# Optimization experiments

Hardware: AMD Instinct MI355X
Metric: run time of the kernel (lower is better)

Reference implementation:

```python
import jax, jax.numpy as jnp
import numpy as np

N, E = 50000, 500000
IN_C, HID, OUT_C, HEADS, NL = 128, 16, 16, 8, 4
EPS = 1e-5
NEG_SLOPE = 0.2


def _gatv2(x, src, dst, Wl, Wr, att, bias, concat):
    # GATv2Conv (PyG semantics, eval mode): lin_l on source, lin_r on target,
    # e = a . LeakyReLU(xl[src] + xr[dst]); segment softmax over dst; scatter-sum.
    n = x.shape[0]
    H, C = att.shape
    xl = (x @ Wl).reshape(n, H, C)
    xr = (x @ Wr).reshape(n, H, C)
    e = jax.nn.leaky_relu(xl[src] + xr[dst], NEG_SLOPE)          # [E', H, C]
    logit = jnp.einsum('ehc,hc->eh', e, att)                      # [E', H]
    mx = jax.lax.stop_gradient(jax.ops.segment_max(logit, dst, num_segments=n))
    a = jnp.exp(logit - mx[dst])
    denom = jax.ops.segment_sum(a, dst, num_segments=n)
    alpha = a / denom[dst]                                        # [E', H]
    out = jax.ops.segment_sum(xl[src] * alpha[..., None], dst, num_segments=n)
    out = out.reshape(n, H * C) if concat else out.mean(axis=1)
    return out + bias


def _bn_eval(x, g, b, m, v):
    return (x - m) * jax.lax.rsqrt(v + EPS) * g + b


def setup_inputs() -> dict:
    key = jax.random.key(0)
    ks = jax.random.split(key, 32)
    d = {}
    d['x'] = jax.random.normal(ks[0], (N, IN_C), dtype=jnp.float32)
    d['edge_index'] = jax.random.randint(ks[1], (2, E), 0, N, dtype=jnp.int64)
    HC = HID * HEADS  # 128
    dims_in = [IN_C, HC, HC, HC]
    dims_h = [HEADS, HEADS, HEADS, 1]
    dims_c = [HID, HID, HID, OUT_C]
    ki = 2
    for i in range(NL):
        fan = dims_in[i]
        s = 1.0 / np.sqrt(fan)
        d[f'W{i}l'] = jax.random.uniform(ks[ki], (fan, dims_h[i] * dims_c[i]), minval=-s, maxval=s, dtype=jnp.float32); ki += 1
        d[f'W{i}r'] = jax.random.uniform(ks[ki], (fan, dims_h[i] * dims_c[i]), minval=-s, maxval=s, dtype=jnp.float32); ki += 1
        d[f'a{i}'] = jax.random.normal(ks[ki], (dims_h[i], dims_c[i]), dtype=jnp.float32) * 0.1; ki += 1
        out_dim = dims_h[i] * dims_c[i] if i < NL - 1 else dims_c[i]
        d[f'b{i}'] = jnp.zeros((out_dim,), dtype=jnp.float32)
    for i in range(NL - 1):
        d[f'g{i}'] = jnp.ones((HC,), dtype=jnp.float32) + 0.1 * jax.random.normal(ks[ki], (HC,), dtype=jnp.float32); ki += 1
        d[f'be{i}'] = 0.1 * jax.random.normal(ks[ki], (HC,), dtype=jnp.float32); ki += 1
        d[f'm{i}'] = 0.1 * jax.random.normal(ks[ki], (HC,), dtype=jnp.float32); ki += 1
        d[f'v{i}'] = jnp.ones((HC,), dtype=jnp.float32)
    return d


def reference(x, edge_index, W0l, W0r, a0, b0, W1l, W1r, a1, b1, W2l, W2r, a2, b2, W3l, W3r, a3, b3, g0, be0, m0, v0, g1, be1, m1, v1, g2, be2, m2, v2):
    n = x.shape[0]
    loop = jnp.arange(n, dtype=edge_index.dtype)
    src = jnp.concatenate([edge_index[0], loop])  # add_self_loops=True (PyG default)
    dst = jnp.concatenate([edge_index[1], loop])
    Ws = [(W0l, W0r, a0, b0), (W1l, W1r, a1, b1), (W2l, W2r, a2, b2), (W3l, W3r, a3, b3)]
    bns = [(g0, be0, m0, v0), (g1, be1, m1, v1), (g2, be2, m2, v2)]
    h = x
    for i in range(NL):
        Wl, Wr, att, bias = Ws[i]
        h = _gatv2(h, src, dst, Wl, Wr, att, bias, concat=(i < NL - 1))
        if i < NL - 1:
            g, b, m, v = bns[i]
            h = jax.nn.elu(_bn_eval(h, g, b, m, v))
    return h
```

## Files before the change

kernel.cpp:

```cpp
#include <hip/hip_runtime.h>
#include <hip/hip_fp16.h>
#include <math.h>

static constexpr float BN_EPS = 1e-5f;
static constexpr float NEG = 0.2f;

typedef float f32x4 __attribute__((ext_vector_type(4)));
typedef _Float16 h16x2 __attribute__((ext_vector_type(2)));
typedef _Float16 h16x8 __attribute__((ext_vector_type(8)));


__global__ void hist_kernel(const int* __restrict__ ei, int E, int n, int* __restrict__ cnt) {
    int e = blockIdx.x * blockDim.x + threadIdx.x;
    int ET = E + n;
    if (e >= ET) return;
    int d = (e < E) ? ei[E + e] : (e - E);
    atomicAdd(&cnt[d], 1);
}

__global__ void scan_block(const int* __restrict__ cnt, int* __restrict__ rowptr,
                           int* __restrict__ bsums, int n) {
    __shared__ int s[1024];
    int i = blockIdx.x * 1024 + threadIdx.x;
    int vv = (i < n) ? cnt[i] : 0;
    s[threadIdx.x] = vv;
    __syncthreads();
    for (int d = 1; d < 1024; d <<= 1) {
        int t = (threadIdx.x >= d) ? s[threadIdx.x - d] : 0;
        __syncthreads();
        s[threadIdx.x] += t;
        __syncthreads();
    }
    if (i < n) rowptr[i + 1] = s[threadIdx.x];
    if (threadIdx.x == 1023) bsums[blockIdx.x] = s[1023];
}

__global__ void scan_bsums(int* __restrict__ bsums, int nb) {
    int L = threadIdx.x;
    int v = (L < nb) ? bsums[L] : 0;
    for (int d = 1; d < 64; d <<= 1) {
        int t = __shfl_up(v, d);
        if (L >= d) v += t;
    }
    int ex = __shfl_up(v, 1);
    if (L == 0) ex = 0;
    if (L < nb) bsums[L] = ex;
}

__global__ void scan_add(int* __restrict__ rowptr, const int* __restrict__ bsums, int n) {
    int i = blockIdx.x * 1024 + threadIdx.x;
    if (i < n) rowptr[i + 1] += bsums[blockIdx.x];
    if (i == 0) rowptr[0] = 0;
}

__global__ void scatter_kernel(const int* __restrict__ ei, int E, int n,
                               const int* __restrict__ rowptr, int* __restrict__ fill,
                               int* __restrict__ col) {
    int e = blockIdx.x * blockDim.x + threadIdx.x;
    int ET = E + n;
    if (e >= ET) return;
    int s, d;
    if (e < E) { s = ei[e]; d = ei[E + e]; } else { s = e - E; d = s; }
    int pos = atomicAdd(&fill[d], 1);
    col[rowptr[d] + pos] = s;
}


__global__ void pack_all(const float* __restrict__ W0l, const float* __restrict__ W0r,
                         const float* __restrict__ W1l, const float* __restrict__ W1r,
                         const float* __restrict__ W2l, const float* __restrict__ W2r,
                         const float* __restrict__ W3l, const float* __restrict__ W3r,
                         __half* __restrict__ pk0, __half* __restrict__ pk1,
                         __half* __restrict__ pk2, __half* __restrict__ pk3) {
    int b = blockIdx.x;
    const float *Wl, *Wr;
    __half* packed;
    int tile, NTT, M;
    if (b < 192) {
        int layer = b >> 6;
        tile = b & 63;
        NTT = 16; M = 128;
        Wl = (layer == 0) ? W0l : (layer == 1) ? W1l : W2l;
        Wr = (layer == 0) ? W0r : (layer == 1) ? W1r : W2r;
        packed = (layer == 0) ? pk0 : (layer == 1) ? pk1 : pk2;
    } else {
        tile = b - 192;
        NTT = 2; M = 16;
        Wl = W3l; Wr = W3r; packed = pk3;
    }
    int NT = NTT >> 1;
    int gnt = tile % NTT;
    int kt = tile / NTT;
    int l = threadIdx.x;
    const float* W = (gnt < NT) ? Wl : Wr;
    int col = (gnt % NT) * 16 + (l & 15);
    int krow = kt * 32 + ((l >> 4) << 3);
    size_t base = (size_t)tile * 512 + (size_t)l * 8;
#pragma unroll
    for (int j = 0; j < 8; j++)
        packed[base + j] = __float2half(W[(size_t)(krow + j) * M + col]);
}


template <bool FIRST>
__global__ __launch_bounds__(256) void gemm_h_big(
    const __half* __restrict__ xh, const float* __restrict__ xf,
    const __half* __restrict__ packed,
    __half* __restrict__ Y1, __half* __restrict__ Y2, int n) {
    __shared__ _Float16 sA[64 * 136];
    const int t = threadIdx.x;
    const int row0 = blockIdx.x * 64;

    for (int c = t; c < 1024; c += 256) {
        int row = c >> 4;
        int off = (c & 15) * 8;
        int gr = row0 + row;
        if (gr >= n) gr = n - 1;
        if (FIRST) {
            float4 v0 = *(const float4*)&xf[(size_t)gr * 128 + off];
            float4 v1 = *(const float4*)&xf[(size_t)gr * 128 + off + 4];
            h16x8 h = {(_Float16)v0.x, (_Float16)v0.y, (_Float16)v0.z, (_Float16)v0.w,
                       (_Float16)v1.x, (_Float16)v1.y, (_Float16)v1.z, (_Float16)v1.w};
            *(h16x8*)&sA[row * 136 + off] = h;
        } else {
            *(h16x8*)&sA[row * 136 + off] = *(const h16x8*)&xh[(size_t)gr * 128 + off];
        }
    }
    __syncthreads();

    const int lane = t & 63;
    const int s = t >> 6;
    const int lr = lane & 15;
    const int kq = (lane >> 4) * 8;

    h16x8 af[4][4];
#pragma unroll
    for (int rt = 0; rt < 4; rt++)
#pragma unroll
        for (int kt = 0; kt < 4; kt++)
            af[rt][kt] = *(const h16x8*)&sA[(rt * 16 + lr) * 136 + kt * 32 + kq];

    f32x4 acc[4][4];
#pragma unroll
    for (int a = 0; a < 4; a++)
#pragma unroll
        for (int b = 0; b < 4; b++) acc[a][b] = (f32x4){0.f, 0.f, 0.f, 0.f};

#pragma unroll
    for (int kt = 0; kt < 4; kt++) {
#pragma unroll
        for (int ntl = 0; ntl < 4; ntl++) {
            int nt = s * 4 + ntl;
            h16x8 b = *(const h16x8*)&packed[((size_t)(kt * 16 + nt)) * 512 + lane * 8];
#pragma unroll
            for (int rt = 0; rt < 4; rt++)
                acc[ntl][rt] = __builtin_amdgcn_mfma_f32_16x16x32_f16(af[rt][kt], b, acc[ntl][rt], 0, 0, 0);
        }
    }

    __half* Y = (s < 2) ? Y1 : Y2;
    const int colh = (s & 1) * 64;
    const int rq = (lane >> 4) * 4;
#pragma unroll
    for (int ntl = 0; ntl < 4; ntl++) {
        int col = colh + ntl * 16 + lr;
#pragma unroll
        for (int rt = 0; rt < 4; rt++) {
#pragma unroll
            for (int g = 0; g < 4; g++) {
                int row = row0 + rt * 16 + rq + g;
                if (row < n) Y[(size_t)row * 128 + col] = __float2half(acc[ntl][rt][g]);
            }
        }
    }
}


__global__ __launch_bounds__(256) void gemm_h_small(
    const __half* __restrict__ xh, const __half* __restrict__ packed,
    float* __restrict__ Y1, float* __restrict__ Y2, int n) {
    int lane = threadIdx.x & 63;
    int wv = blockIdx.x * 4 + (threadIdx.x >> 6);
    int row0 = wv * 16;
    if (row0 >= n) return;
    int r = row0 + (lane & 15);
    if (r >= n) r = n - 1;
    int kq = (lane >> 4) * 8;

    h16x8 af[4];
#pragma unroll
    for (int kt = 0; kt < 4; kt++)
        af[kt] = *(const h16x8*)&xh[(size_t)r * 128 + kt * 32 + kq];

    f32x4 acc[2];
    acc[0] = (f32x4){0.f, 0.f, 0.f, 0.f};
    acc[1] = (f32x4){0.f, 0.f, 0.f, 0.f};

#pragma unroll
    for (int kt = 0; kt < 4; kt++) {
#pragma unroll
        for (int nt = 0; nt < 2; nt++) {
            h16x8 b = *(const h16x8*)&packed[((size_t)(kt * 2 + nt)) * 512 + lane * 8];
            acc[nt] = __builtin_amdgcn_mfma_f32_16x16x32_f16(af[kt], b, acc[nt], 0, 0, 0);
        }
    }

    int colb = lane & 15;
    int rbase = row0 + (lane >> 4) * 4;
#pragma unroll
    for (int nt = 0; nt < 2; nt++) {
        float* Y = (nt == 0) ? Y1 : Y2;
#pragma unroll
        for (int g = 0; g < 4; g++) {
            int row = rbase + g;
            if (row < n) Y[(size_t)row * 16 + colb] = acc[nt][g];
        }
    }
}


__device__ __forceinline__ float dot4_h(h16x2 l01, h16x2 l23,
                                        h16x2 a01, h16x2 a23) {
#if __has_builtin(__builtin_amdgcn_fdot2)
    float part = __builtin_amdgcn_fdot2(l01, a01, 0.f, false);
    return __builtin_amdgcn_fdot2(l23, a23, part, false);
#else
    return fmaf((float)l01.x, (float)a01.x, fmaf((float)l01.y, (float)a01.y,
           fmaf((float)l23.x, (float)a23.x, (float)l23.y * (float)a23.y)));
#endif
}

__global__ __launch_bounds__(256) void agg_h(
    const __half* __restrict__ xl, const __half* __restrict__ xr,
    const int* __restrict__ rowptr, const int* __restrict__ col,
    const float* __restrict__ att, const float* __restrict__ bias,
    const float* __restrict__ g, const float* __restrict__ be,
    const float* __restrict__ bm, const float* __restrict__ bv,
    __half* __restrict__ oh, int n) {
    int v = (blockIdx.x * blockDim.x + threadIdx.x) >> 6;
    if (v >= n) return;
    int lane = threadIdx.x & 63;
    int half = lane >> 5;
    int L = lane & 31;
    int ch = 4 * L;

    float2 rraw = *(const float2*)&xr[(size_t)v * 128 + ch];
    h16x2 rx01 = *(h16x2*)&rraw.x;
    h16x2 rx23 = *(h16x2*)&rraw.y;
    float4 av = *(const float4*)&att[ch];
    h16x2 a01 = {(_Float16)av.x, (_Float16)av.y};
    h16x2 a23 = {(_Float16)av.z, (_Float16)av.w};
    const h16x2 neg2 = {(_Float16)NEG, (_Float16)NEG};

    int beg = rowptr[v];
    int end = rowptr[v + 1];

    float lrun = 0.f;
    float4 acc = make_float4(0.f, 0.f, 0.f, 0.f);

    auto proc = [&](float2 raw, bool ok) {
        h16x2 h01 = *(h16x2*)&raw.x;
        h16x2 h23 = *(h16x2*)&raw.y;
        h16x2 s01 = h01 + rx01;
        h16x2 s23 = h23 + rx23;
        h16x2 l01 = __builtin_elementwise_max(s01, s01 * neg2);
        h16x2 l23 = __builtin_elementwise_max(s23, s23 * neg2);
        float part = dot4_h(l01, l23, a01, a23);
        part += __shfl_xor(part, 1);
        part += __shfl_xor(part, 2);
        float p = ok ? __expf(part) : 0.f;
        lrun += p;
        acc.x = fmaf(p, (float)h01.x, acc.x);
        acc.y = fmaf(p, (float)h01.y, acc.y);
        acc.z = fmaf(p, (float)h23.x, acc.z);
        acc.w = fmaf(p, (float)h23.y, acc.w);
    };

    int e = beg;
    for (; e + 8 <= end; e += 8) {
        float2 r[4];
#pragma unroll
        for (int j = 0; j < 4; j++) {
            int u = col[e + 2 * j + half];
            r[j] = *(const float2*)&xl[((size_t)u << 7) + ch];
        }
#pragma unroll
        for (int j = 0; j < 4; j++) proc(r[j], true);
    }
    for (; e < end; e += 4) {
        float2 r[2];
        bool ok[2];
#pragma unroll
        for (int j = 0; j < 2; j++) {
            int idx = e + 2 * j + half;
            ok[j] = (idx < end);
            r[j] = make_float2(0.f, 0.f);
            if (ok[j]) {
                int u = col[idx];
                r[j] = *(const float2*)&xl[((size_t)u << 7) + ch];
            }
        }
#pragma unroll
        for (int j = 0; j < 2; j++) proc(r[j], ok[j]);
    }

    lrun += __shfl_xor(lrun, 32);
    acc.x += __shfl_xor(acc.x, 32);
    acc.y += __shfl_xor(acc.y, 32);
    acc.z += __shfl_xor(acc.z, 32);
    acc.w += __shfl_xor(acc.w, 32);

    if (half == 0) {
        float inv = 1.0f / lrun;
        float4 b4 = *(const float4*)&bias[ch];
        float o[4] = {fmaf(acc.x, inv, b4.x), fmaf(acc.y, inv, b4.y),
                      fmaf(acc.z, inv, b4.z), fmaf(acc.w, inv, b4.w)};
        float4 m4 = *(const float4*)&bm[ch];
        float4 v4 = *(const float4*)&bv[ch];
        float4 g4 = *(const float4*)&g[ch];
        float4 e4 = *(const float4*)&be[ch];
        float ms[4] = {m4.x, m4.y, m4.z, m4.w};
        float vs[4] = {v4.x, v4.y, v4.z, v4.w};
        float gs[4] = {g4.x, g4.y, g4.z, g4.w};
        float es[4] = {e4.x, e4.y, e4.z, e4.w};
        unsigned short h[4];
#pragma unroll
        for (int j = 0; j < 4; j++) {
            o[j] = (o[j] - ms[j]) * rsqrtf(vs[j] + BN_EPS) * gs[j] + es[j];
            o[j] = o[j] > 0.f ? o[j] : expm1f(o[j]);
            h[j] = __half_as_ushort(__float2half(o[j]));
        }
        *(ushort4*)&oh[(size_t)v * 128 + ch] = make_ushort4(h[0], h[1], h[2], h[3]);
    }
}


__global__ __launch_bounds__(256) void agg_f(
    const float* __restrict__ xl, const float* __restrict__ xr,
    const int* __restrict__ rowptr, const int* __restrict__ col,
    const float* __restrict__ att, const float* __restrict__ bias,
    float* __restrict__ out, int n) {
    int v = (blockIdx.x * blockDim.x + threadIdx.x) >> 6;
    if (v >= n) return;
    int lane = threadIdx.x & 63;
    int slot = lane >> 2;
    int L = lane & 3;
    int ch = 4 * L;

    float4 xrv = *(const float4*)&xr[(size_t)v * 16 + ch];
    float4 av = *(const float4*)&att[ch];
    int beg = rowptr[v];
    int end = rowptr[v + 1];

    float lrun = 0.f;
    float4 acc = make_float4(0.f, 0.f, 0.f, 0.f);

    for (int eb = beg; eb < end; eb += 16) {
        int idx = eb + slot;
        bool ok = (idx < end);
        float4 xv = make_float4(0.f, 0.f, 0.f, 0.f);
        if (ok) {
            int u = col[idx];
            xv = *(const float4*)&xl[((size_t)u << 4) + ch];
        }
        float s0 = xv.x + xrv.x; s0 = s0 > 0.f ? s0 : NEG * s0;
        float s1 = xv.y + xrv.y; s1 = s1 > 0.f ? s1 : NEG * s1;
        float s2 = xv.z + xrv.z; s2 = s2 > 0.f ? s2 : NEG * s2;
        float s3 = xv.w + xrv.w; s3 = s3 > 0.f ? s3 : NEG * s3;
        float part = fmaf(s0, av.x, fmaf(s1, av.y, fmaf(s2, av.z, s3 * av.w)));
        part += __shfl_xor(part, 1);
        part += __shfl_xor(part, 2);
        float p = ok ? __expf(part) : 0.f;
        lrun += p;
        acc.x = fmaf(p, xv.x, acc.x);
        acc.y = fmaf(p, xv.y, acc.y);
        acc.z = fmaf(p, xv.z, acc.z);
        acc.w = fmaf(p, xv.w, acc.w);
    }

#pragma unroll
    for (int d = 4; d < 64; d <<= 1) {
        lrun += __shfl_xor(lrun, d);
        acc.x += __shfl_xor(acc.x, d);
        acc.y += __shfl_xor(acc.y, d);
        acc.z += __shfl_xor(acc.z, d);
        acc.w += __shfl_xor(acc.w, d);
    }

    if (slot == 0) {
        float inv = 1.0f / lrun;
        float4 b4 = *(const float4*)&bias[ch];
        *(float4*)&out[(size_t)v * 16 + ch] =
            make_float4(fmaf(acc.x, inv, b4.x), fmaf(acc.y, inv, b4.y),
                        fmaf(acc.z, inv, b4.z), fmaf(acc.w, inv, b4.w));
    }
}


extern "C" void kernel_launch(void* const* d_in, const int* in_sizes, int n_in,
                              void* d_out, int out_size, void* d_ws, size_t ws_size,
                              hipStream_t stream) {
    const float* x = (const float*)d_in[0];
    const int* ei = (const int*)d_in[1];
    const float* Wl[4] = {(const float*)d_in[2], (const float*)d_in[6],
                          (const float*)d_in[10], (const float*)d_in[14]};
    const float* Wr[4] = {(const float*)d_in[3], (const float*)d_in[7],
                          (const float*)d_in[11], (const float*)d_in[15]};
    const float* att[4] = {(const float*)d_in[4], (const float*)d_in[8],
                           (const float*)d_in[12], (const float*)d_in[16]};
    const float* bias[4] = {(const float*)d_in[5], (const float*)d_in[9],
                            (const float*)d_in[13], (const float*)d_in[17]};
    const float* g[3] = {(const float*)d_in[18], (const float*)d_in[22], (const float*)d_in[26]};
    const float* be[3] = {(const float*)d_in[19], (const float*)d_in[23], (const float*)d_in[27]};
    const float* bm[3] = {(const float*)d_in[20], (const float*)d_in[24], (const float*)d_in[28]};
    const float* bv[3] = {(const float*)d_in[21], (const float*)d_in[25], (const float*)d_in[29]};

    const int n = in_sizes[0] / 128;
    const int E = in_sizes[1] / 2;
    const int ET = E + n;

    char* p = (char*)d_ws;
    __half* xh = (__half*)p;           p += (size_t)n * 128 * 2;
    __half* xlh = (__half*)p;          p += (size_t)n * 128 * 2;
    __half* xrh = (__half*)p;          p += (size_t)n * 128 * 2;
    float* xl3 = (float*)p;            p += (size_t)n * 16 * 4;
    float* xr3 = (float*)p;            p += (size_t)n * 16 * 4;
    int* rowptr = (int*)p;            p += (size_t)(n + 1) * 4;
    int* cnt = (int*)p;               p += (size_t)n * 4;
    int* fill = (int*)p;              p += (size_t)n * 4;
    int* col = (int*)p;               p += (size_t)ET * 4;
    int* bsums = (int*)p;             p += 256;
    __half* pk[4];
    for (int i = 0; i < 3; i++) { pk[i] = (__half*)p; p += 4 * 16 * 512 * 2; }
    pk[3] = (__half*)p;               p += 4 * 2 * 512 * 2;

    (void)hipMemsetAsync(cnt, 0, (size_t)n * 4, stream);
    (void)hipMemsetAsync(fill, 0, (size_t)n * 4, stream);

    const int tb = 256;
    hist_kernel<<<(ET + tb - 1) / tb, tb, 0, stream>>>(ei, E, n, cnt);
    int nb = (n + 1023) / 1024;
    scan_block<<<nb, 1024, 0, stream>>>(cnt, rowptr, bsums, n);
    scan_bsums<<<1, 64, 0, stream>>>(bsums, nb);
    scan_add<<<nb, 1024, 0, stream>>>(rowptr, bsums, n);
    scatter_kernel<<<(ET + tb - 1) / tb, tb, 0, stream>>>(ei, E, n, rowptr, fill, col);

    pack_all<<<200, 64, 0, stream>>>(Wl[0], Wr[0], Wl[1], Wr[1], Wl[2], Wr[2],
                                     Wl[3], Wr[3], pk[0], pk[1], pk[2], pk[3]);

    const int gb64 = (n + 63) / 64;
    const int gemmBlocksSmall = ((n + 15) / 16 + 3) / 4;
    const int aggBlocks = (n + 3) / 4;

    gemm_h_big<true><<<gb64, 256, 0, stream>>>(nullptr, x, pk[0], xlh, xrh, n);
    agg_h<<<aggBlocks, 256, 0, stream>>>(
        xlh, xrh, rowptr, col, att[0], bias[0], g[0], be[0], bm[0], bv[0], xh, n);
    for (int i = 1; i < 3; i++) {
        gemm_h_big<false><<<gb64, 256, 0, stream>>>(xh, nullptr, pk[i], xlh, xrh, n);
        agg_h<<<aggBlocks, 256, 0, stream>>>(
            xlh, xrh, rowptr, col, att[i], bias[i], g[i], be[i], bm[i], bv[i], xh, n);
    }
    gemm_h_small<<<gemmBlocksSmall, 256, 0, stream>>>(xh, pk[3], xl3, xr3, n);
    agg_f<<<aggBlocks, 256, 0, stream>>>(
        xl3, xr3, rowptr, col, att[3], bias[3], (float*)d_out, n);
}
```

Baseline: 372.9 us.

## Fuse CSR construction into one cooperative kernel with grid syncs

Replaces the two memsets and five separate CSR-building kernels (histogram, block scan, bsum scan, scan add, scatter) with a single cooperative kernel that uses grid-wide syncs between phases. The goal is to remove per-launch overhead and inter-kernel gaps in the graph preprocessing. In exchange it adds grid.sync barriers and a persistent grid sized by occupancy, which may run with less parallelism than the original launches. It also assumes at most 256 scan chunks (n up to 65536), since the second-level scan only covers 256 entries.

New measurement: 1.279 ms. 3.43x slower.

```diff
diff --git a/kernel.cpp b/kernel.cpp
--- a/kernel.cpp
+++ b/kernel.cpp
@@ -1,6 +1,9 @@
 #include <hip/hip_runtime.h>
 #include <hip/hip_fp16.h>
+#include <hip/hip_cooperative_groups.h>
 #include <math.h>
+
+namespace cg = cooperative_groups;
 
 static constexpr float BN_EPS = 1e-5f;
 static constexpr float NEG = 0.2f;
@@ -10,59 +13,68 @@
 typedef _Float16 h16x8 __attribute__((ext_vector_type(8)));
 
 
-__global__ void hist_kernel(const int* __restrict__ ei, int E, int n, int* __restrict__ cnt) {
-    int e = blockIdx.x * blockDim.x + threadIdx.x;
-    int ET = E + n;
-    if (e >= ET) return;
-    int d = (e < E) ? ei[E + e] : (e - E);
-    atomicAdd(&cnt[d], 1);
-}
-
-__global__ void scan_block(const int* __restrict__ cnt, int* __restrict__ rowptr,
-                           int* __restrict__ bsums, int n) {
-    __shared__ int s[1024];
-    int i = blockIdx.x * 1024 + threadIdx.x;
-    int vv = (i < n) ? cnt[i] : 0;
-    s[threadIdx.x] = vv;
-    __syncthreads();
-    for (int d = 1; d < 1024; d <<= 1) {
-        int t = (threadIdx.x >= d) ? s[threadIdx.x - d] : 0;
+__global__ __launch_bounds__(256) void csr_build(
+    const int* __restrict__ ei, int E, int n,
+    int* __restrict__ cnt, int* __restrict__ fill,
+    int* __restrict__ rowptr, int* __restrict__ col,
+    int* __restrict__ bsums, int nc) {
+    cg::grid_group grid = cg::this_grid();
+    const int tid = blockIdx.x * blockDim.x + threadIdx.x;
+    const int nthreads = gridDim.x * blockDim.x;
+    const int ET = E + n;
+    __shared__ int s[256];
+
+    for (int i = tid; i < n; i += nthreads) { cnt[i] = 0; fill[i] = 0; }
+    grid.sync();
+
+    for (int e = tid; e < ET; e += nthreads) {
+        int d = (e < E) ? ei[E + e] : (e - E);
+        atomicAdd(&cnt[d], 1);
+    }
+    grid.sync();
+
+    for (int c = blockIdx.x; c < nc; c += gridDim.x) {
+        int i = c * 256 + threadIdx.x;
+        int v = (i < n) ? cnt[i] : 0;
+        s[threadIdx.x] = v;
         __syncthreads();
-        s[threadIdx.x] += t;
+        for (int d = 1; d < 256; d <<= 1) {
+            int t = (threadIdx.x >= d) ? s[threadIdx.x - d] : 0;
+            __syncthreads();
+            s[threadIdx.x] += t;
+            __syncthreads();
+        }
+        if (i < n) rowptr[i + 1] = s[threadIdx.x];
+        if (threadIdx.x == 255) bsums[c] = s[255];
         __syncthreads();
     }
-    if (i < n) rowptr[i + 1] = s[threadIdx.x];
-    if (threadIdx.x == 1023) bsums[blockIdx.x] = s[1023];
-}
-
-__global__ void scan_bsums(int* __restrict__ bsums, int nb) {
-    int L = threadIdx.x;
-    int v = (L < nb) ? bsums[L] : 0;
-    for (int d = 1; d < 64; d <<= 1) {
-        int t = __shfl_up(v, d);
-        if (L >= d) v += t;
-    }
-    int ex = __shfl_up(v, 1);
-    if (L == 0) ex = 0;
-    if (L < nb) bsums[L] = ex;
-}
-
-__global__ void scan_add(int* __restrict__ rowptr, const int* __restrict__ bsums, int n) {
-    int i = blockIdx.x * 1024 + threadIdx.x;
-    if (i < n) rowptr[i + 1] += bsums[blockIdx.x];
-    if (i == 0) rowptr[0] = 0;
-}
-
-__global__ void scatter_kernel(const int* __restrict__ ei, int E, int n,
-                               const int* __restrict__ rowptr, int* __restrict__ fill,
-                               int* __restrict__ col) {
-    int e = blockIdx.x * blockDim.x + threadIdx.x;
-    int ET = E + n;
-    if (e >= ET) return;
-    int s, d;
-    if (e < E) { s = ei[e]; d = ei[E + e]; } else { s = e - E; d = s; }
-    int pos = atomicAdd(&fill[d], 1);
-    col[rowptr[d] + pos] = s;
+    grid.sync();
+
+    if (blockIdx.x == 0) {
+        int L = threadIdx.x;
+        s[L] = (L < nc) ? bsums[L] : 0;
+        __syncthreads();
+        for (int d = 1; d < 256; d <<= 1) {
+            int t = (L >= d) ? s[L - d] : 0;
+            __syncthreads();
+            s[L] += t;
+            __syncthreads();
+        }
+        int ex = (L == 0) ? 0 : s[L - 1];
+        if (L < nc) bsums[L] = ex;
+    }
+    grid.sync();
+
+    for (int i = tid; i < n; i += nthreads) rowptr[i + 1] += bsums[i >> 8];
+    if (tid == 0) rowptr[0] = 0;
+    grid.sync();
+
+    for (int e = tid; e < ET; e += nthreads) {
+        int sv, d;
+        if (e < E) { sv = ei[e]; d = ei[E + e]; } else { sv = e - E; d = sv; }
+        int pos = atomicAdd(&fill[d], 1);
+        col[rowptr[d] + pos] = sv;
+    }
 }
 
 
@@ -429,21 +441,22 @@
     int* cnt = (int*)p;               p += (size_t)n * 4;
     int* fill = (int*)p;              p += (size_t)n * 4;
     int* col = (int*)p;               p += (size_t)ET * 4;
-    int* bsums = (int*)p;             p += 256;
+    int* bsums = (int*)p;             p += 1024;
     __half* pk[4];
     for (int i = 0; i < 3; i++) { pk[i] = (__half*)p; p += 4 * 16 * 512 * 2; }
     pk[3] = (__half*)p;               p += 4 * 2 * 512 * 2;
 
-    (void)hipMemsetAsync(cnt, 0, (size_t)n * 4, stream);
-    (void)hipMemsetAsync(fill, 0, (size_t)n * 4, stream);
-
-    const int tb = 256;
-    hist_kernel<<<(ET + tb - 1) / tb, tb, 0, stream>>>(ei, E, n, cnt);
-    int nb = (n + 1023) / 1024;
-    scan_block<<<nb, 1024, 0, stream>>>(cnt, rowptr, bsums, n);
-    scan_bsums<<<1, 64, 0, stream>>>(bsums, nb);
-    scan_add<<<nb, 1024, 0, stream>>>(rowptr, bsums, n);
-    scatter_kernel<<<(ET + tb - 1) / tb, tb, 0, stream>>>(ei, E, n, rowptr, fill, col);
+    int nc = (n + 255) / 256;
+    int blocksPerCU = 0;
+    (void)hipOccupancyMaxActiveBlocksPerMultiprocessor(&blocksPerCU, (const void*)csr_build, 256, 0);
+    if (blocksPerCU < 1) blocksPerCU = 1;
+    int csrGrid = blocksPerCU * 256;
+    if (csrGrid > 2048) csrGrid = 2048;
+    int E_ = E, n_ = n, nc_ = nc;
+    void* args[] = {(void*)&ei, (void*)&E_, (void*)&n_, (void*)&cnt, (void*)&fill,
+                    (void*)&rowptr, (void*)&col, (void*)&bsums, (void*)&nc_};
+    (void)hipLaunchCooperativeKernel((const void*)csr_build, dim3(csrGrid), dim3(256),
+                                     args, 0, stream);
 
     pack_all<<<200, 64, 0, stream>>>(Wl[0], Wr[0], Wl[1], Wr[1], Wl[2], Wr[2],
                                      Wl[3], Wr[3], pk[0], pk[1], pk[2], pk[3]);
```
